# Kernel optimization log

Hardware: AMD Instinct MI355X
Metric: run time of the kernel (lower is better)

## Reference

```python
import jax, jax.numpy as jnp
import numpy as np

N_NODES = 50000
N_GRAPHS = 128


def gcn_conv(x, edge_index, W, b, n_nodes):
    # PyG GCNConv: h = D^{-1/2}(A+I)D^{-1/2} (x W) + b
    h = x @ W  # [N, H]
    loop = jnp.arange(n_nodes)
    src = jnp.concatenate([edge_index[0], loop])
    dst = jnp.concatenate([edge_index[1], loop])
    deg = jax.ops.segment_sum(jnp.ones_like(dst, h.dtype), dst, num_segments=n_nodes)
    dinv = jnp.where(deg > 0, deg ** -0.5, 0.0)
    norm = dinv[src] * dinv[dst]  # [E+N]
    msgs = h[src] * norm[:, None]  # gather + normalize
    out = jax.ops.segment_sum(msgs, dst, num_segments=n_nodes)  # scatter-add
    return out + b


def setup_inputs() -> dict:
    key = jax.random.key(0)
    ks = jax.random.split(key, 8)
    F_in, H, L = 128, 128, 7
    x = jax.random.normal(ks[0], (N_NODES, F_in), dtype=jnp.float32)
    edge_index = jax.random.randint(ks[1], (2, 800000), 0, N_NODES, dtype=jnp.int64)
    batch = jnp.sort(jax.random.randint(ks[2], (N_NODES,), 0, N_GRAPHS, dtype=jnp.int64))
    s = lambda f: (1.0 / np.sqrt(f)).astype(np.float32)
    W1 = jax.random.normal(ks[3], (F_in, H), dtype=jnp.float32) * s(F_in)
    b1 = jnp.zeros((H,), jnp.float32)
    W2 = jax.random.normal(ks[4], (H, H), dtype=jnp.float32) * s(H)
    b2 = jnp.zeros((H,), jnp.float32)
    Wfc = jax.random.normal(ks[5], (H, L), dtype=jnp.float32) * s(H)
    bfc = jnp.zeros((L,), jnp.float32)
    return {"x": x, "edge_index": edge_index, "batch": batch,
            "W1": W1, "b1": b1, "W2": W2, "b2": b2, "Wfc": Wfc, "bfc": bfc}


def reference(x, edge_index, batch, W1, b1, W2, b2, Wfc, bfc):
    n = x.shape[0]
    h = jax.nn.relu(gcn_conv(x, edge_index, W1, b1, n))
    h = jax.nn.relu(gcn_conv(h, edge_index, W2, b2, n))
    # global_mean_pool over batch vector
    sums = jax.ops.segment_sum(h, batch, num_segments=N_GRAPHS)  # [G, H]
    cnt = jax.ops.segment_sum(jnp.ones((n,), h.dtype), batch, num_segments=N_GRAPHS)
    pooled = sums / jnp.maximum(cnt, 1.0)[:, None]
    return pooled @ Wfc + bfc  # [G, label_dim]
```

## Files before the change

kernel.cpp:

```cpp
#include <hip/hip_runtime.h>
#include <hip/hip_bf16.h>

#define HD 128
#define NL 7
#define BCAP 6144

typedef __attribute__((ext_vector_type(8))) short bf16x8;
typedef __attribute__((ext_vector_type(4))) float f32x4;

__device__ __forceinline__ unsigned short f2bf(float f) {
    __hip_bfloat16 b = __float2bfloat16(f);
    return *reinterpret_cast<unsigned short*>(&b);
}
__device__ __forceinline__ float bf2f(unsigned short u) {
    unsigned int x = ((unsigned int)u) << 16;
    return __uint_as_float(x);
}


__global__ __launch_bounds__(256) void k_prep(int* __restrict__ gbcur, int nb,
                                              float* __restrict__ sums, int m,
                                              const float* __restrict__ W1,
                                              const float* __restrict__ W2,
                                              unsigned short* __restrict__ Wt1,
                                              unsigned short* __restrict__ Wt2) {
    int i = blockIdx.x * 256 + threadIdx.x;
    if (i < nb) gbcur[i] = 0;
    if (i < m) sums[i] = 0.f;
    if (i < HD * HD) {
        int k = i >> 7, nn = i & 127;
        Wt1[nn * HD + k] = f2bf(W1[i]);
        Wt2[nn * HD + k] = f2bf(W2[i]);
    }
}


__global__ __launch_bounds__(256) void k_bucket(const int* __restrict__ src,
                                                const int* __restrict__ dst, int E,
                                                int* __restrict__ gbcur,
                                                int* __restrict__ stage, int nb) {
    __shared__ int lh[256];
    __shared__ int gb[256];
    int t = threadIdx.x;
    if (t < nb) lh[t] = 0;
    __syncthreads();

    int e0 = blockIdx.x * 4096;
    int bk[16]; int lr[16]; int rec[16];
    #pragma unroll
    for (int j = 0; j < 16; ++j) {
        int e = e0 + j * 256 + t;
        if (e < E) {
            int d = dst[e];
            int s = src[e];
            bk[j]  = d >> 8;
            rec[j] = ((d & 255) << 16) | s;
            lr[j]  = atomicAdd(&lh[bk[j]], 1);
        } else {
            bk[j] = -1; lr[j] = 0; rec[j] = 0;
        }
    }
    __syncthreads();
    if (t < nb) gb[t] = atomicAdd(&gbcur[t], lh[t]);
    __syncthreads();
    #pragma unroll
    for (int j = 0; j < 16; ++j) {
        if (bk[j] >= 0) {
            int p = gb[bk[j]] + lr[j];
            if (p < BCAP) stage[bk[j] * BCAP + p] = rec[j];
        }
    }
}


__global__ __launch_bounds__(256) void k_build(const int* __restrict__ stage,
                                               const int* __restrict__ gbcnt,
                                               int* __restrict__ col,
                                               int* __restrict__ row_start,
                                               float* __restrict__ dinv, int n, int nb) {
    __shared__ int rec_s[BCAP];
    __shared__ unsigned short rank_s[BCAP];
    __shared__ int hist[256];
    __shared__ int scan_s[256];
    int b = blockIdx.x, t = threadIdx.x;

    int cval = (t < nb) ? gbcnt[t] : 0;
    scan_s[t] = cval;
    __syncthreads();
    #pragma unroll
    for (int off = 1; off < 256; off <<= 1) {
        int v = (t >= off) ? scan_s[t - off] : 0;
        __syncthreads();
        scan_s[t] += v;
        __syncthreads();
    }
    __shared__ int base_s;
    if (t == b) base_s = scan_s[t] - cval;
    if (b == 0 && t == 0) row_start[n] = scan_s[nb - 1];
    __syncthreads();
    int base = base_s;
    int cnt  = min(gbcnt[b], BCAP);
    int node0 = b << 8;

    hist[t] = 0;
    __syncthreads();
    for (int e = t; e < cnt; e += 256) {
        int r = stage[b * BCAP + e];
        rec_s[e] = r;
        rank_s[e] = (unsigned short)atomicAdd(&hist[r >> 16], 1);
    }
    __syncthreads();

    int deg = hist[t];
    int node = node0 + t;
    if (node < n) dinv[node] = 1.0f / sqrtf((float)(deg + 1));

    scan_s[t] = deg;
    __syncthreads();
    #pragma unroll
    for (int off = 1; off < 256; off <<= 1) {
        int v = (t >= off) ? scan_s[t - off] : 0;
        __syncthreads();
        scan_s[t] += v;
        __syncthreads();
    }
    int lrs = scan_s[t] - deg;
    hist[t] = lrs;
    if (node < n) row_start[node] = base + lrs;
    __syncthreads();

    for (int e = t; e < cnt; e += 256) {
        int r = rec_s[e];
        col[base + hist[r >> 16] + rank_s[e]] = r & 0xFFFF;
    }
}


template <typename TIN>
__global__ __launch_bounds__(256) void k_gemm_mfma(const TIN* __restrict__ X,
                                                   const unsigned short* __restrict__ Wt,
                                                   unsigned short* __restrict__ Y, int n) {
    int wave = threadIdx.x >> 6, lane = threadIdx.x & 63;
    int lm = lane & 15, g = lane >> 4;
    int m0 = blockIdx.x * 64 + wave * 16;
    int row = m0 + lm;
    bool rok = row < n;

    f32x4 acc[8] = {};

    #pragma unroll
    for (int kb = 0; kb < 4; ++kb) {
        int k0 = kb * 32 + g * 8;
        bf16x8 a = {0, 0, 0, 0, 0, 0, 0, 0};
        if (rok) {
            if constexpr (sizeof(TIN) == 4) {
                const float* xp = (const float*)X + (size_t)row * HD + k0;
                float4 v0 = *(const float4*)xp;
                float4 v1 = *(const float4*)(xp + 4);
                a[0] = (short)f2bf(v0.x); a[1] = (short)f2bf(v0.y);
                a[2] = (short)f2bf(v0.z); a[3] = (short)f2bf(v0.w);
                a[4] = (short)f2bf(v1.x); a[5] = (short)f2bf(v1.y);
                a[6] = (short)f2bf(v1.z); a[7] = (short)f2bf(v1.w);
            } else {
                a = *(const bf16x8*)((const unsigned short*)X + (size_t)row * HD + k0);
            }
        }
        #pragma unroll
        for (int nt = 0; nt < 8; ++nt) {
            int ncol = nt * 16 + lm;
            bf16x8 bfrag = *(const bf16x8*)(Wt + (size_t)ncol * HD + k0);
            acc[nt] = __builtin_amdgcn_mfma_f32_16x16x32_bf16(a, bfrag, acc[nt], 0, 0, 0);
        }
    }

    #pragma unroll
    for (int nt = 0; nt < 8; ++nt) {
        #pragma unroll
        for (int r = 0; r < 4; ++r) {
            int orow = m0 + g * 4 + r;
            if (orow < n) Y[(size_t)orow * HD + nt * 16 + lm] = f2bf(acc[nt][r]);
        }
    }
}


__global__ __launch_bounds__(256) void k_agg(const unsigned short* __restrict__ hin,
                                             const float* __restrict__ dinv,
                                             const int* __restrict__ row_start,
                                             const int* __restrict__ col,
                                             const float* __restrict__ bias,
                                             unsigned short* __restrict__ hout, int n) {
    int wave = threadIdx.x >> 6;
    int lane = threadIdx.x & 63;
    int v = blockIdx.x * 4 + wave;
    if (v >= n) return;

    int h  = lane >> 5;
    int li = lane & 31;
    int f  = li * 4;

    float dv = dinv[v];
    float a0 = 0.f, a1 = 0.f, a2 = 0.f, a3 = 0.f;

    int e  = row_start[v];
    int e1 = row_start[v + 1];

    for (; e + 8 <= e1; e += 8) {
        int s0 = col[e + h];
        int s1 = col[e + h + 2];
        int s2 = col[e + h + 4];
        int s3 = col[e + h + 6];
        float w0 = dinv[s0] * dv, w1 = dinv[s1] * dv;
        float w2 = dinv[s2] * dv, w3 = dinv[s3] * dv;
        ushort4 r0 = *(const ushort4*)(hin + (size_t)s0 * HD + f);
        ushort4 r1 = *(const ushort4*)(hin + (size_t)s1 * HD + f);
        ushort4 r2 = *(const ushort4*)(hin + (size_t)s2 * HD + f);
        ushort4 r3 = *(const ushort4*)(hin + (size_t)s3 * HD + f);
        a0 = fmaf(bf2f(r0.x), w0, a0); a1 = fmaf(bf2f(r0.y), w0, a1);
        a2 = fmaf(bf2f(r0.z), w0, a2); a3 = fmaf(bf2f(r0.w), w0, a3);
        a0 = fmaf(bf2f(r1.x), w1, a0); a1 = fmaf(bf2f(r1.y), w1, a1);
        a2 = fmaf(bf2f(r1.z), w1, a2); a3 = fmaf(bf2f(r1.w), w1, a3);
        a0 = fmaf(bf2f(r2.x), w2, a0); a1 = fmaf(bf2f(r2.y), w2, a1);
        a2 = fmaf(bf2f(r2.z), w2, a2); a3 = fmaf(bf2f(r2.w), w2, a3);
        a0 = fmaf(bf2f(r3.x), w3, a0); a1 = fmaf(bf2f(r3.y), w3, a1);
        a2 = fmaf(bf2f(r3.z), w3, a2); a3 = fmaf(bf2f(r3.w), w3, a3);
    }

    {
        #pragma unroll
        for (int j = 0; j < 4; ++j) {
            int idx = e + h + 2 * j;
            if (idx < e1) {
                int s = col[idx];
                float w = dinv[s] * dv;
                ushort4 r = *(const ushort4*)(hin + (size_t)s * HD + f);
                a0 = fmaf(bf2f(r.x), w, a0); a1 = fmaf(bf2f(r.y), w, a1);
                a2 = fmaf(bf2f(r.z), w, a2); a3 = fmaf(bf2f(r.w), w, a3);
            }
        }
    }

    a0 += __shfl_xor(a0, 32);
    a1 += __shfl_xor(a1, 32);
    a2 += __shfl_xor(a2, 32);
    a3 += __shfl_xor(a3, 32);

    if (h == 0) {
        ushort4 sv = *(const ushort4*)(hin + (size_t)v * HD + f);
        float selfw = dv * dv;
        float4 b = *(const float4*)(bias + f);
        ushort4 o;
        o.x = f2bf(fmaxf(fmaf(bf2f(sv.x), selfw, a0) + b.x, 0.f));
        o.y = f2bf(fmaxf(fmaf(bf2f(sv.y), selfw, a1) + b.y, 0.f));
        o.z = f2bf(fmaxf(fmaf(bf2f(sv.z), selfw, a2) + b.z, 0.f));
        o.w = f2bf(fmaxf(fmaf(bf2f(sv.w), selfw, a3) + b.w, 0.f));
        __builtin_nontemporal_store(*(unsigned long long*)&o,
            (unsigned long long*)(hout + (size_t)v * HD + f));
    }
}


#define POOL_ROWS 32

__global__ __launch_bounds__(128) void k_pool_partial(const unsigned short* __restrict__ h,
                                                      const int* __restrict__ batch,
                                                      float* __restrict__ sums, int n) {
    __shared__ int bs[POOL_ROWS];
    int t = threadIdx.x;
    int r0 = blockIdx.x * POOL_ROWS;
    int r1 = min(r0 + POOL_ROWS, n);
    int cnt = r1 - r0;
    if (t < cnt) bs[t] = batch[r0 + t];
    __syncthreads();

    int g = bs[0];
    float acc = 0.f;
    for (int i = 0; i < cnt; ++i) {
        int bg = bs[i];
        if (bg != g) {
            atomicAdd(&sums[(size_t)g * HD + t], acc);
            acc = 0.f;
            g = bg;
        }
        acc += bf2f(h[(size_t)(r0 + i) * HD + t]);
    }
    atomicAdd(&sums[(size_t)g * HD + t], acc);
}


__global__ __launch_bounds__(128) void k_fc(const float* __restrict__ sums,
                                            const int* __restrict__ batch,
                                            const float* __restrict__ Wfc,
                                            const float* __restrict__ bfc,
                                            float* __restrict__ out, int n) {
    int g = blockIdx.x;
    int t = threadIdx.x;
    __shared__ int slo, shi;
    if (t == 0) {
        int lo = 0, hi = n;
        while (lo < hi) { int m = (lo + hi) >> 1; if (batch[m] < g) lo = m + 1; else hi = m; }
        slo = lo;
        lo = 0; hi = n;
        while (lo < hi) { int m = (lo + hi) >> 1; if (batch[m] < g + 1) lo = m + 1; else hi = m; }
        shi = lo;
    }
    __syncthreads();
    float cnt = (float)(shi - slo);
    __shared__ float sp[HD];
    sp[t] = sums[(size_t)g * HD + t] / fmaxf(cnt, 1.f);
    __syncthreads();
    if (t < NL) {
        float o = bfc[t];
        for (int k = 0; k < HD; ++k) o = fmaf(sp[k], Wfc[k * NL + t], o);
        out[g * NL + t] = o;
    }
}


extern "C" void kernel_launch(void* const* d_in, const int* in_sizes, int n_in,
                              void* d_out, int out_size, void* d_ws, size_t ws_size,
                              hipStream_t stream) {
    const float* x    = (const float*)d_in[0];
    const int*   ei   = (const int*)d_in[1];
    const int*   batch= (const int*)d_in[2];
    const float* W1   = (const float*)d_in[3];
    const float* b1   = (const float*)d_in[4];
    const float* W2   = (const float*)d_in[5];
    const float* b2   = (const float*)d_in[6];
    const float* Wfc  = (const float*)d_in[7];
    const float* bfc  = (const float*)d_in[8];
    float* out = (float*)d_out;

    int n = in_sizes[0] / HD;
    int E = in_sizes[1] / 2;
    int G = out_size / NL;
    const int* srcp = ei;
    const int* dstp = ei + E;

    int nb = (n + 255) >> 8;

    char* ws = (char*)d_ws;
    auto align256 = [](size_t v) { return (v + 255) & ~(size_t)255; };
    size_t o = 0;
    int*   row_start = (int*)(ws + o); o = align256(o + (size_t)(n + 1) * 4);
    int*   gbcur     = (int*)(ws + o); o = align256(o + (size_t)nb * 4);
    float* dinv      = (float*)(ws + o); o = align256(o + (size_t)n * 4);
    int*   col       = (int*)(ws + o); o = align256(o + (size_t)E * 4);
    unsigned short* tmp  = (unsigned short*)(ws + o); o = align256(o + (size_t)n * HD * 2);
    unsigned short* tmp2 = (unsigned short*)(ws + o); o = align256(o + (size_t)n * HD * 2);
    int*   stage     = (int*)(ws + o); o = align256(o + (size_t)nb * BCAP * 4);
    float* sums      = (float*)(ws + o); o = align256(o + (size_t)G * HD * 4);
    unsigned short* Wt1 = (unsigned short*)(ws + o); o = align256(o + (size_t)HD * HD * 2);
    unsigned short* Wt2 = (unsigned short*)(ws + o); o = align256(o + (size_t)HD * HD * 2);

    int mZero = G * HD;
    k_prep<<<(HD * HD + 255) / 256, 256, 0, stream>>>(gbcur, nb, sums, mZero,
                                                      W1, W2, Wt1, Wt2);

    int nblkC = (E + 4095) / 4096;
    k_bucket<<<nblkC, 256, 0, stream>>>(srcp, dstp, E, gbcur, stage, nb);
    k_build <<<nb, 256, 0, stream>>>(stage, gbcur, col, row_start, dinv, n, nb);

    k_gemm_mfma<float><<<(n + 63) / 64, 256, 0, stream>>>(x, Wt1, tmp, n);
    k_agg<<<(n + 3) / 4, 256, 0, stream>>>(tmp, dinv, row_start, col, b1, tmp2, n);
    k_gemm_mfma<unsigned short><<<(n + 63) / 64, 256, 0, stream>>>(tmp2, Wt2, tmp, n);
    k_agg<<<(n + 3) / 4, 256, 0, stream>>>(tmp, dinv, row_start, col, b2, tmp2, n);

    k_pool_partial<<<(n + POOL_ROWS - 1) / POOL_ROWS, 128, 0, stream>>>(tmp2, batch, sums, n);
    k_fc<<<G, 128, 0, stream>>>(sums, batch, Wfc, bfc, out, n);
}
```

Before: 185.4 us.

## Merge CSR build and first GEMM into one launch to overlap them

```diff
diff --git a/kernel.cpp b/kernel.cpp
--- a/kernel.cpp
+++ b/kernel.cpp
@@ -73,98 +73,128 @@
 }
 
 
-__global__ __launch_bounds__(256) void k_build(const int* __restrict__ stage,
-                                               const int* __restrict__ gbcnt,
-                                               int* __restrict__ col,
-                                               int* __restrict__ row_start,
-                                               float* __restrict__ dinv, int n, int nb) {
+__global__ __launch_bounds__(256) void k_build_gemm1(
+        const int* __restrict__ stage, const int* __restrict__ gbcnt,
+        int* __restrict__ col, int* __restrict__ row_start,
+        float* __restrict__ dinv,
+        const float* __restrict__ X, const unsigned short* __restrict__ Wt,
+        unsigned short* __restrict__ Y, int n, int nb) {
     __shared__ int rec_s[BCAP];
     __shared__ unsigned short rank_s[BCAP];
     __shared__ int hist[256];
     __shared__ int scan_s[256];
-    int b = blockIdx.x, t = threadIdx.x;
-
-    int cval = (t < nb) ? gbcnt[t] : 0;
-    scan_s[t] = cval;
-    __syncthreads();
-    #pragma unroll
-    for (int off = 1; off < 256; off <<= 1) {
-        int v = (t >= off) ? scan_s[t - off] : 0;
-        __syncthreads();
-        scan_s[t] += v;
-        __syncthreads();
-    }
     __shared__ int base_s;
-    if (t == b) base_s = scan_s[t] - cval;
-    if (b == 0 && t == 0) row_start[n] = scan_s[nb - 1];
-    __syncthreads();
-    int base = base_s;
-    int cnt  = min(gbcnt[b], BCAP);
-    int node0 = b << 8;
-
-    hist[t] = 0;
-    __syncthreads();
-    for (int e = t; e < cnt; e += 256) {
-        int r = stage[b * BCAP + e];
-        rec_s[e] = r;
-        rank_s[e] = (unsigned short)atomicAdd(&hist[r >> 16], 1);
-    }
-    __syncthreads();
-
-    int deg = hist[t];
-    int node = node0 + t;
-    if (node < n) dinv[node] = 1.0f / sqrtf((float)(deg + 1));
-
-    scan_s[t] = deg;
-    __syncthreads();
-    #pragma unroll
-    for (int off = 1; off < 256; off <<= 1) {
-        int v = (t >= off) ? scan_s[t - off] : 0;
-        __syncthreads();
-        scan_s[t] += v;
-        __syncthreads();
-    }
-    int lrs = scan_s[t] - deg;
-    hist[t] = lrs;
-    if (node < n) row_start[node] = base + lrs;
-    __syncthreads();
-
-    for (int e = t; e < cnt; e += 256) {
-        int r = rec_s[e];
-        col[base + hist[r >> 16] + rank_s[e]] = r & 0xFFFF;
-    }
-}
-
-
-template <typename TIN>
-__global__ __launch_bounds__(256) void k_gemm_mfma(const TIN* __restrict__ X,
-                                                   const unsigned short* __restrict__ Wt,
-                                                   unsigned short* __restrict__ Y, int n) {
-    int wave = threadIdx.x >> 6, lane = threadIdx.x & 63;
-    int lm = lane & 15, g = lane >> 4;
-    int m0 = blockIdx.x * 64 + wave * 16;
-    int row = m0 + lm;
-    bool rok = row < n;
-
-    f32x4 acc[8] = {};
-
-    #pragma unroll
-    for (int kb = 0; kb < 4; ++kb) {
-        int k0 = kb * 32 + g * 8;
-        bf16x8 a = {0, 0, 0, 0, 0, 0, 0, 0};
-        if (rok) {
-            if constexpr (sizeof(TIN) == 4) {
-                const float* xp = (const float*)X + (size_t)row * HD + k0;
+    int t = threadIdx.x;
+
+    if ((int)blockIdx.x < nb) {
+        int b = blockIdx.x;
+
+        int cval = (t < nb) ? gbcnt[t] : 0;
+        scan_s[t] = cval;
+        __syncthreads();
+        #pragma unroll
+        for (int off = 1; off < 256; off <<= 1) {
+            int v = (t >= off) ? scan_s[t - off] : 0;
+            __syncthreads();
+            scan_s[t] += v;
+            __syncthreads();
+        }
+        if (t == b) base_s = scan_s[t] - cval;
+        if (b == 0 && t == 0) row_start[n] = scan_s[nb - 1];
+        __syncthreads();
+        int base = base_s;
+        int cnt  = min(gbcnt[b], BCAP);
+        int node0 = b << 8;
+
+        hist[t] = 0;
+        __syncthreads();
+        for (int e = t; e < cnt; e += 256) {
+            int r = stage[b * BCAP + e];
+            rec_s[e] = r;
+            rank_s[e] = (unsigned short)atomicAdd(&hist[r >> 16], 1);
+        }
+        __syncthreads();
+
+        int deg = hist[t];
+        int node = node0 + t;
+        if (node < n) dinv[node] = 1.0f / sqrtf((float)(deg + 1));
+
+        scan_s[t] = deg;
+        __syncthreads();
+        #pragma unroll
+        for (int off = 1; off < 256; off <<= 1) {
+            int v = (t >= off) ? scan_s[t - off] : 0;
+            __syncthreads();
+            scan_s[t] += v;
+            __syncthreads();
+        }
+        int lrs = scan_s[t] - deg;
+        hist[t] = lrs;
+        if (node < n) row_start[node] = base + lrs;
+        __syncthreads();
+
+        for (int e = t; e < cnt; e += 256) {
+            int r = rec_s[e];
+            col[base + hist[r >> 16] + rank_s[e]] = r & 0xFFFF;
+        }
+    } else {
+        int wave = t >> 6, lane = t & 63;
+        int lm = lane & 15, g = lane >> 4;
+        int m0 = ((int)blockIdx.x - nb) * 64 + wave * 16;
+        int row = m0 + lm;
+        bool rok = row < n;
+
+        f32x4 acc[8] = {};
+
+        #pragma unroll
+        for (int kb = 0; kb < 4; ++kb) {
+            int k0 = kb * 32 + g * 8;
+            bf16x8 a = {0, 0, 0, 0, 0, 0, 0, 0};
+            if (rok) {
+                const float* xp = X + (size_t)row * HD + k0;
                 float4 v0 = *(const float4*)xp;
                 float4 v1 = *(const float4*)(xp + 4);
                 a[0] = (short)f2bf(v0.x); a[1] = (short)f2bf(v0.y);
                 a[2] = (short)f2bf(v0.z); a[3] = (short)f2bf(v0.w);
                 a[4] = (short)f2bf(v1.x); a[5] = (short)f2bf(v1.y);
                 a[6] = (short)f2bf(v1.z); a[7] = (short)f2bf(v1.w);
-            } else {
-                a = *(const bf16x8*)((const unsigned short*)X + (size_t)row * HD + k0);
             }
-        }
+            #pragma unroll
+            for (int nt = 0; nt < 8; ++nt) {
+                int ncol = nt * 16 + lm;
+                bf16x8 bfrag = *(const bf16x8*)(Wt + (size_t)ncol * HD + k0);
+                acc[nt] = __builtin_amdgcn_mfma_f32_16x16x32_bf16(a, bfrag, acc[nt], 0, 0, 0);
+            }
+        }
+
+        #pragma unroll
+        for (int nt = 0; nt < 8; ++nt) {
+            #pragma unroll
+            for (int r = 0; r < 4; ++r) {
+                int orow = m0 + g * 4 + r;
+                if (orow < n) Y[(size_t)orow * HD + nt * 16 + lm] = f2bf(acc[nt][r]);
+            }
+        }
+    }
+}
+
+
+__global__ __launch_bounds__(256) void k_gemm_mfma_bf(const unsigned short* __restrict__ X,
+                                                      const unsigned short* __restrict__ Wt,
+                                                      unsigned short* __restrict__ Y, int n) {
+    int wave = threadIdx.x >> 6, lane = threadIdx.x & 63;
+    int lm = lane & 15, g = lane >> 4;
+    int m0 = blockIdx.x * 64 + wave * 16;
+    int row = m0 + lm;
+    bool rok = row < n;
+
+    f32x4 acc[8] = {};
+
+    #pragma unroll
+    for (int kb = 0; kb < 4; ++kb) {
+        int k0 = kb * 32 + g * 8;
+        bf16x8 a = {0, 0, 0, 0, 0, 0, 0, 0};
+        if (rok) a = *(const bf16x8*)(X + (size_t)row * HD + k0);
         #pragma unroll
         for (int nt = 0; nt < 8; ++nt) {
             int ncol = nt * 16 + lm;
@@ -359,11 +389,13 @@
 
     int nblkC = (E + 4095) / 4096;
     k_bucket<<<nblkC, 256, 0, stream>>>(srcp, dstp, E, gbcur, stage, nb);
-    k_build <<<nb, 256, 0, stream>>>(stage, gbcur, col, row_start, dinv, n, nb);
-
-    k_gemm_mfma<float><<<(n + 63) / 64, 256, 0, stream>>>(x, Wt1, tmp, n);
+
+    int gemmBlocks = (n + 63) / 64;
+    k_build_gemm1<<<nb + gemmBlocks, 256, 0, stream>>>(stage, gbcur, col, row_start,
+                                                       dinv, x, Wt1, tmp, n, nb);
+
     k_agg<<<(n + 3) / 4, 256, 0, stream>>>(tmp, dinv, row_start, col, b1, tmp2, n);
-    k_gemm_mfma<unsigned short><<<(n + 63) / 64, 256, 0, stream>>>(tmp2, Wt2, tmp, n);
+    k_gemm_mfma_bf<<<gemmBlocks, 256, 0, stream>>>(tmp2, Wt2, tmp, n);
     k_agg<<<(n + 3) / 4, 256, 0, stream>>>(tmp, dinv, row_start, col, b2, tmp2, n);
 
     k_pool_partial<<<(n + POOL_ROWS - 1) / POOL_ROWS, 128, 0, stream>>>(tmp2, batch, sums, n);
```

New measurement: 174.1 us. 1.06x faster.
